# Kernel optimization log

Hardware: AMD Instinct MI355X
Metric: run time of the kernel (lower is better)

The kernel has to match this reference:

```python
import jax, jax.numpy as jnp
import numpy as np

N_E = 16384
E_DIM = 8
BETA = 0.25


def setup_inputs() -> dict:
    key = jax.random.key(0)
    k1, k2 = jax.random.split(key)
    z = jax.random.normal(k1, (4, E_DIM, 64, 64), dtype=jnp.float32)
    # nn.Embedding init: uniform(-1/n_e, 1/n_e)
    emb = jax.random.uniform(k2, (N_E, E_DIM), dtype=jnp.float32,
                             minval=-1.0 / N_E, maxval=1.0 / N_E)
    return {"z": z, "emb": emb}


def reference(z, emb):
    # z: [B, C, H, W] with C == e_dim; emb: [n_e, e_dim]
    zt = jnp.transpose(z, (0, 2, 3, 1))            # b h w c
    zf = zt.reshape(-1, E_DIM)                     # [N, e_dim]
    # squared distances: ||z||^2 + ||e||^2 - 2 z.e -> [N, n_e]
    d = (jnp.sum(zf * zf, axis=1, keepdims=True)
         + jnp.sum(emb * emb, axis=1)
         - 2.0 * jnp.einsum('nd,kd->nk', zf, emb))
    idx = jnp.argmin(d, axis=1)                    # [N]
    z_q = emb[idx].reshape(zt.shape)               # b h w c
    sg = jax.lax.stop_gradient
    # legacy loss: mean((sg(z_q)-z)^2) + beta*mean((z_q-sg(z))^2)
    loss = jnp.mean((sg(z_q) - zt) ** 2) + BETA * jnp.mean((z_q - sg(zt)) ** 2)
    # straight-through estimator
    z_q = zt + sg(z_q - zt)
    z_q = jnp.transpose(z_q, (0, 3, 1, 2))         # b c h w
    return z_q, loss, idx
```

## Files before the change

kernel.cpp:

```cpp
#include <hip/hip_runtime.h>


typedef short bf16x8  __attribute__((ext_vector_type(8)));
typedef float f32x16  __attribute__((ext_vector_type(16)));
typedef float f32x2   __attribute__((ext_vector_type(2)));

#define N_ROW 16384
#define N_E   16384
#define NSPL  32
#define SPLIT (N_E / NSPL)
#define ITER  (SPLIT / 32)
#define FIN_BLOCKS (N_ROW / 256)

static __device__ __forceinline__ unsigned short bf16_rne(float x) {
    unsigned u = __float_as_uint(x);
    unsigned r = (u >> 16) & 1u;
    return (unsigned short)((u + 0x7FFFu + r) >> 16);
}

__global__ __launch_bounds__(256) void vq_prep(const float* __restrict__ z,
                                               const float* __restrict__ emb,
                                               unsigned short* __restrict__ pz,
                                               unsigned short* __restrict__ pe_hi,
                                               float* __restrict__ Zn_arr,
                                               unsigned long long* __restrict__ key,
                                               double* __restrict__ acc,
                                               unsigned* __restrict__ done) {
    const int t = blockIdx.x * 256 + threadIdx.x;
    if (t < N_ROW) {
        const int b = t >> 12, hw = t & 4095;
        const float* zp = z + (size_t)b * 32768 + hw;
        float v[8];
#pragma unroll
        for (int c = 0; c < 8; ++c) v[c] = zp[c * 4096];
        float Zn;
        {
#pragma clang fp contract(off)
            Zn = v[0] * v[0];
#pragma unroll
            for (int c = 1; c < 8; ++c) { float q = v[c] * v[c]; Zn = Zn + q; }
        }
        unsigned hb[8], lb[8];
#pragma unroll
        for (int c = 0; c < 8; ++c) {
            hb[c] = bf16_rne(v[c]);
            float hf = __uint_as_float(hb[c] << 16);
            lb[c] = bf16_rne(v[c] - hf);
        }
        uint4 uh, ul;
        uh.x = hb[0] | (hb[1] << 16); uh.y = hb[2] | (hb[3] << 16);
        uh.z = hb[4] | (hb[5] << 16); uh.w = hb[6] | (hb[7] << 16);
        ul.x = lb[0] | (lb[1] << 16); ul.y = lb[2] | (lb[3] << 16);
        ul.z = lb[4] | (lb[5] << 16); ul.w = lb[6] | (lb[7] << 16);
        ((uint4*)pz)[(size_t)t * 2]     = uh;
        ((uint4*)pz)[(size_t)t * 2 + 1] = ul;
        Zn_arr[t] = Zn;
        key[t] = ~0ull;
        if (t == 0) { *acc = 0.0; *done = 0u; }
    } else {
        const int k = t - N_ROW;
        const float* e = emb + (size_t)k * 8;
        unsigned hb[8];
#pragma unroll
        for (int c = 0; c < 8; ++c) hb[c] = bf16_rne(e[c]);
        uint4 uh;
        uh.x = hb[0] | (hb[1] << 16); uh.y = hb[2] | (hb[3] << 16);
        uh.z = hb[4] | (hb[5] << 16); uh.w = hb[6] | (hb[7] << 16);
        ((uint4*)pe_hi)[k] = uh;
    }
}

__global__ __launch_bounds__(256, 4) void vq_maxk(const unsigned short* __restrict__ pe_hi,
                                                  const unsigned short* __restrict__ pz,
                                                  float* __restrict__ maxs) {
    __shared__ __align__(16) unsigned short se_hi[SPLIT * 8];
    const int tid = threadIdx.x, wid = tid >> 6, lane = tid & 63;
    const int rowbase = (int)(blockIdx.x >> 5) * 256;
    const int split = blockIdx.x & 31;
    const int c32 = lane & 31, hi = lane >> 5;

    bf16x8 afrag[2];
#pragma unroll
    for (int a = 0; a < 2; ++a)
        afrag[a] = *(const bf16x8*)(pz + (size_t)(rowbase + wid * 64 + a * 32 + c32) * 16 + hi * 8);

    {
        const uint4* gh = (const uint4*)(pe_hi + (size_t)split * SPLIT * 8);
        ((uint4*)se_hi)[tid]       = gh[tid];
        ((uint4*)se_hi)[tid + 256] = gh[tid + 256];
    }
    __syncthreads();

    const f32x16 zero16 = {0.f,0.f,0.f,0.f,0.f,0.f,0.f,0.f,0.f,0.f,0.f,0.f,0.f,0.f,0.f,0.f};
    f32x2 rmax2[2][8];
#pragma unroll
    for (int a = 0; a < 2; ++a)
#pragma unroll
        for (int j = 0; j < 8; ++j) rmax2[a][j] = (f32x2){-3.4e38f, -3.4e38f};

#pragma unroll 2
    for (int t = 0; t < ITER; ++t) {
        const bf16x8 bfrag = *(const bf16x8*)(se_hi + (size_t)(t * 32 + c32) * 8);
        f32x16 cc0 = __builtin_amdgcn_mfma_f32_32x32x16_bf16(afrag[0], bfrag, zero16, 0, 0, 0);
        f32x16 cc1 = __builtin_amdgcn_mfma_f32_32x32x16_bf16(afrag[1], bfrag, zero16, 0, 0, 0);
#pragma unroll
        for (int j = 0; j < 8; ++j) {
            rmax2[0][j] = __builtin_elementwise_max(rmax2[0][j], (f32x2){cc0[2*j], cc0[2*j+1]});
            rmax2[1][j] = __builtin_elementwise_max(rmax2[1][j], (f32x2){cc1[2*j], cc1[2*j+1]});
        }
    }
#pragma unroll
    for (int a = 0; a < 2; ++a)
#pragma unroll
        for (int reg = 0; reg < 16; ++reg) {
            float m = rmax2[a][reg >> 1][reg & 1];
            m = fmaxf(m, __shfl_xor(m, 1));
            m = fmaxf(m, __shfl_xor(m, 2));
            m = fmaxf(m, __shfl_xor(m, 4));
            m = fmaxf(m, __shfl_xor(m, 8));
            m = fmaxf(m, __shfl_xor(m, 16));
            if (c32 == 0) {
                const int row = rowbase + wid * 64 + a * 32 + (reg & 3) + 8 * (reg >> 2) + 4 * hi;
                maxs[(size_t)split * N_ROW + row] = m;
            }
        }
}

__global__ __launch_bounds__(256) void vq_thr(const float* __restrict__ maxs,
                                              const float* __restrict__ Zn_arr,
                                              float* __restrict__ thr) {
    const int row = blockIdx.x * 256 + threadIdx.x;
    float m = -3.4e38f;
#pragma unroll
    for (int s = 0; s < NSPL; ++s) m = fmaxf(m, maxs[(size_t)s * N_ROW + row]);
    const float Zn = Zn_arr[row];
    const float W = __builtin_fmaf(Zn, 1.5e-7f, __builtin_fmaf(__builtin_sqrtf(Zn), 6.8e-7f, 2e-7f));
    thr[row] = m - W;
}

__global__ __launch_bounds__(256, 4) void vq_coll(const float* __restrict__ z,
                                                  const float* __restrict__ emb,
                                                  const unsigned short* __restrict__ pe_hi,
                                                  const unsigned short* __restrict__ pz,
                                                  const float* __restrict__ Zn_arr,
                                                  const float* __restrict__ thr_arr,
                                                  unsigned long long* __restrict__ key) {
    __shared__ __align__(16) unsigned short se_hi[SPLIT * 8];
    __shared__ float se_z[8 * 256];
    __shared__ float sZn[256], sthr[256];
    const int tid = threadIdx.x, wid = tid >> 6, lane = tid & 63;
    const int rowbase = (int)(blockIdx.x >> 5) * 256;
    const int split = blockIdx.x & 31;
    const int c32 = lane & 31, hi = lane >> 5;

    bf16x8 afrag[2];
#pragma unroll
    for (int a = 0; a < 2; ++a)
        afrag[a] = *(const bf16x8*)(pz + (size_t)(rowbase + wid * 64 + a * 32 + c32) * 16 + hi * 8);

    {
        const uint4* gh = (const uint4*)(pe_hi + (size_t)split * SPLIT * 8);
        ((uint4*)se_hi)[tid]       = gh[tid];
        ((uint4*)se_hi)[tid + 256] = gh[tid + 256];
        const int row = rowbase + tid;
        const int b = row >> 12, hw = row & 4095;
#pragma unroll
        for (int c = 0; c < 8; ++c)
            se_z[c * 256 + tid] = z[(size_t)b * 32768 + (size_t)c * 4096 + hw];
        sZn[tid]  = Zn_arr[row];
        sthr[tid] = thr_arr[row];
    }
    __syncthreads();

    f32x2 thr2[2][8];
#pragma unroll
    for (int a = 0; a < 2; ++a) {
        const int base = wid * 64 + a * 32 + 4 * hi;
#pragma unroll
        for (int j = 0; j < 8; ++j) {
            const int r0 = base + ((2 * j) & 3) + 8 * (j >> 1);
            thr2[a][j] = (f32x2){sthr[r0], sthr[r0 + 1]};
        }
    }

    const f32x16 zero16 = {0.f,0.f,0.f,0.f,0.f,0.f,0.f,0.f,0.f,0.f,0.f,0.f,0.f,0.f,0.f,0.f};
#pragma unroll 2
    for (int t = 0; t < ITER; ++t) {
        const bf16x8 bfrag = *(const bf16x8*)(se_hi + (size_t)(t * 32 + c32) * 8);
        f32x16 cc0 = __builtin_amdgcn_mfma_f32_32x32x16_bf16(afrag[0], bfrag, zero16, 0, 0, 0);
        f32x16 cc1 = __builtin_amdgcn_mfma_f32_32x32x16_bf16(afrag[1], bfrag, zero16, 0, 0, 0);

        f32x2 dd[2][8];
#pragma unroll
        for (int j = 0; j < 8; ++j) {
            dd[0][j] = (f32x2){cc0[2*j], cc0[2*j+1]} - thr2[0][j];
            dd[1][j] = (f32x2){cc1[2*j], cc1[2*j+1]} - thr2[1][j];
        }
        f32x2 mx = dd[0][0];
#pragma unroll
        for (int j = 1; j < 8; ++j) mx = __builtin_elementwise_max(mx, dd[0][j]);
#pragma unroll
        for (int j = 0; j < 8; ++j) mx = __builtin_elementwise_max(mx, dd[1][j]);

        if (__any(fmaxf(mx.x, mx.y) >= 0.f)) {
            const int kcode = split * SPLIT + t * 32 + c32;
#pragma unroll
            for (int a = 0; a < 2; ++a) {
                f32x2 am = dd[a][0];
#pragma unroll
                for (int j = 1; j < 8; ++j) am = __builtin_elementwise_max(am, dd[a][j]);
                if (__any(fmaxf(am.x, am.y) >= 0.f)) {
#pragma unroll
                    for (int j = 0; j < 8; ++j)
#pragma unroll
                        for (int h = 0; h < 2; ++h) {
                            const float dv = dd[a][j][h];
                            if (__any(dv >= 0.f)) {
                                if (dv >= 0.f) {
                                    const int reg = 2 * j + h;
                                    const int lrow = wid * 64 + a * 32 + (reg & 3) + 8 * (reg >> 2) + 4 * hi;
                                    const float* e = emb + (size_t)kcode * 8;
                                    float dot = se_z[lrow] * e[0];
#pragma unroll
                                    for (int c = 1; c < 8; ++c)
                                        dot = __builtin_fmaf(se_z[c * 256 + lrow], e[c], dot);
                                    const float ddv = __builtin_fmaf(-2.f, dot, sZn[lrow]);
                                    unsigned u = __float_as_uint(ddv);
                                    unsigned mm = (u & 0x80000000u) ? ~u : (u | 0x80000000u);
                                    const unsigned long long kk =
                                        ((unsigned long long)mm << 32) | (unsigned)kcode;
                                    atomicMin(&key[(size_t)(rowbase + lrow)], kk);
                                }
                            }
                        }
                }
            }
        }
    }
}

__global__ __launch_bounds__(256) void vq_fin(const float* __restrict__ z,
                                              const float* __restrict__ emb,
                                              const unsigned long long* __restrict__ key,
                                              float* __restrict__ out_zq,
                                              float* __restrict__ out_idx,
                                              double* __restrict__ acc,
                                              unsigned* __restrict__ done,
                                              float* __restrict__ out_loss) {
    __shared__ float red[4];
    const int row = blockIdx.x * 256 + threadIdx.x;
    const int b = row >> 12, hw = row & 4095;
    const int kstar = (int)(unsigned)(key[row] & 0xFFFFFFFFull);
    out_idx[row] = (float)kstar;
    const float* e = emb + (size_t)kstar * 8;
    float s = 0.f;
#pragma unroll
    for (int c = 0; c < 8; ++c) {
        const size_t zoff = (size_t)b * 32768 + (size_t)c * 4096 + hw;
        const float ev = e[c];
        const float df = ev - z[zoff];
        out_zq[zoff] = ev;
        s = __builtin_fmaf(df, df, s);
    }
#pragma unroll
    for (int off = 32; off > 0; off >>= 1) s += __shfl_down(s, off, 64);
    if ((threadIdx.x & 63) == 0) red[threadIdx.x >> 6] = s;
    __syncthreads();
    if (threadIdx.x == 0) {
        double t = (double)red[0] + (double)red[1] + (double)red[2] + (double)red[3];
        atomicAdd(acc, t);
        __threadfence();
        unsigned old = atomicAdd(done, 1u);
        if (old == FIN_BLOCKS - 1) {
            double total = atomicAdd(acc, 0.0);
            float mf = (float)(total / (double)(N_ROW * 8));
            out_loss[0] = mf + 0.25f * mf;
        }
    }
}

extern "C" void kernel_launch(void* const* d_in, const int* in_sizes, int n_in,
                              void* d_out, int out_size, void* d_ws, size_t ws_size,
                              hipStream_t stream) {
    const float* z   = (const float*)d_in[0];
    const float* emb = (const float*)d_in[1];

    float* out      = (float*)d_out;
    float* out_zq   = out;
    float* out_loss = out + 131072;
    float* out_idx  = out + 131073;

    char* w = (char*)d_ws;
    double*             acc   = (double*)w;
    unsigned*           done  = (unsigned*)(w + 8);      w += 64;
    unsigned long long* key   = (unsigned long long*)w;  w += (size_t)N_ROW * 8;
    float*              Zn    = (float*)w;               w += (size_t)N_ROW * 4;
    float*              thr   = (float*)w;               w += (size_t)N_ROW * 4;
    unsigned short*     pz    = (unsigned short*)w;      w += (size_t)N_ROW * 32;
    unsigned short*     pe_hi = (unsigned short*)w;      w += (size_t)N_E * 16;
    float*              maxs  = (float*)w;               w += (size_t)N_ROW * NSPL * 4;

    vq_prep <<<dim3(128), dim3(256), 0, stream>>>(z, emb, pz, pe_hi, Zn, key, acc, done);
    vq_maxk <<<dim3((N_ROW / 256) * NSPL), dim3(256), 0, stream>>>(pe_hi, pz, maxs);
    vq_thr  <<<dim3(N_ROW / 256), dim3(256), 0, stream>>>(maxs, Zn, thr);
    vq_coll <<<dim3((N_ROW / 256) * NSPL), dim3(256), 0, stream>>>(z, emb, pe_hi, pz, Zn, thr, key);
    vq_fin  <<<dim3(FIN_BLOCKS), dim3(256), 0, stream>>>(z, emb, key, out_zq, out_idx, acc, done, out_loss);
}
```

Before: 61.24 us.

## Replace per-split max buffer with atomic max and drop threshold kernel

The max-score kernel now reduces each row's maximum straight into a global array with atomicMax on a monotone unsigned float encoding. This replaces the per-split max array and the separate threshold kernel, and the collection kernel now computes the threshold from the decoded max itself. The finalize kernel is also re-parallelized so each thread handles one output element in z's native layout rather than one row of eight strided elements. The goal is to remove a launch and the round trip of the 2 MB max buffer, at the cost of global atomic contention on the max array.

```diff
diff --git a/kernel.cpp b/kernel.cpp
--- a/kernel.cpp
+++ b/kernel.cpp
@@ -10,12 +10,20 @@
 #define NSPL  32
 #define SPLIT (N_E / NSPL)
 #define ITER  (SPLIT / 32)
-#define FIN_BLOCKS (N_ROW / 256)
+#define FIN_BLOCKS ((N_ROW * 8) / 256)
 
 static __device__ __forceinline__ unsigned short bf16_rne(float x) {
     unsigned u = __float_as_uint(x);
     unsigned r = (u >> 16) & 1u;
     return (unsigned short)((u + 0x7FFFu + r) >> 16);
+}
+static __device__ __forceinline__ unsigned mono_enc(float x) {
+    unsigned u = __float_as_uint(x);
+    return (u & 0x80000000u) ? ~u : (u | 0x80000000u);
+}
+static __device__ __forceinline__ float mono_dec(unsigned g) {
+    unsigned u = (g & 0x80000000u) ? (g & 0x7FFFFFFFu) : ~g;
+    return __uint_as_float(u);
 }
 
 __global__ __launch_bounds__(256) void vq_prep(const float* __restrict__ z,
@@ -23,6 +31,7 @@
                                                unsigned short* __restrict__ pz,
                                                unsigned short* __restrict__ pe_hi,
                                                float* __restrict__ Zn_arr,
+                                               unsigned* __restrict__ gmax,
                                                unsigned long long* __restrict__ key,
                                                double* __restrict__ acc,
                                                unsigned* __restrict__ done) {
@@ -55,6 +64,7 @@
         ((uint4*)pz)[(size_t)t * 2]     = uh;
         ((uint4*)pz)[(size_t)t * 2 + 1] = ul;
         Zn_arr[t] = Zn;
+        gmax[t] = 0u;
         key[t] = ~0ull;
         if (t == 0) { *acc = 0.0; *done = 0u; }
     } else {
@@ -72,7 +82,7 @@
 
 __global__ __launch_bounds__(256, 4) void vq_maxk(const unsigned short* __restrict__ pe_hi,
                                                   const unsigned short* __restrict__ pz,
-                                                  float* __restrict__ maxs) {
+                                                  unsigned* __restrict__ gmax) {
     __shared__ __align__(16) unsigned short se_hi[SPLIT * 8];
     const int tid = threadIdx.x, wid = tid >> 6, lane = tid & 63;
     const int rowbase = (int)(blockIdx.x >> 5) * 256;
@@ -121,21 +131,9 @@
             m = fmaxf(m, __shfl_xor(m, 16));
             if (c32 == 0) {
                 const int row = rowbase + wid * 64 + a * 32 + (reg & 3) + 8 * (reg >> 2) + 4 * hi;
-                maxs[(size_t)split * N_ROW + row] = m;
+                atomicMax(&gmax[row], mono_enc(m));
             }
         }
-}
-
-__global__ __launch_bounds__(256) void vq_thr(const float* __restrict__ maxs,
-                                              const float* __restrict__ Zn_arr,
-                                              float* __restrict__ thr) {
-    const int row = blockIdx.x * 256 + threadIdx.x;
-    float m = -3.4e38f;
-#pragma unroll
-    for (int s = 0; s < NSPL; ++s) m = fmaxf(m, maxs[(size_t)s * N_ROW + row]);
-    const float Zn = Zn_arr[row];
-    const float W = __builtin_fmaf(Zn, 1.5e-7f, __builtin_fmaf(__builtin_sqrtf(Zn), 6.8e-7f, 2e-7f));
-    thr[row] = m - W;
 }
 
 __global__ __launch_bounds__(256, 4) void vq_coll(const float* __restrict__ z,
@@ -143,7 +141,7 @@
                                                   const unsigned short* __restrict__ pe_hi,
                                                   const unsigned short* __restrict__ pz,
                                                   const float* __restrict__ Zn_arr,
-                                                  const float* __restrict__ thr_arr,
+                                                  const unsigned* __restrict__ gmax,
                                                   unsigned long long* __restrict__ key) {
     __shared__ __align__(16) unsigned short se_hi[SPLIT * 8];
     __shared__ float se_z[8 * 256];
@@ -167,8 +165,11 @@
 #pragma unroll
         for (int c = 0; c < 8; ++c)
             se_z[c * 256 + tid] = z[(size_t)b * 32768 + (size_t)c * 4096 + hw];
-        sZn[tid]  = Zn_arr[row];
-        sthr[tid] = thr_arr[row];
+        const float Zn = Zn_arr[row];
+        sZn[tid] = Zn;
+        const float W = __builtin_fmaf(Zn, 1.5e-7f,
+                          __builtin_fmaf(__builtin_sqrtf(Zn), 6.8e-7f, 2e-7f));
+        sthr[tid] = mono_dec(gmax[row]) - W;
     }
     __syncthreads();
 
@@ -225,10 +226,8 @@
                                     for (int c = 1; c < 8; ++c)
                                         dot = __builtin_fmaf(se_z[c * 256 + lrow], e[c], dot);
                                     const float ddv = __builtin_fmaf(-2.f, dot, sZn[lrow]);
-                                    unsigned u = __float_as_uint(ddv);
-                                    unsigned mm = (u & 0x80000000u) ? ~u : (u | 0x80000000u);
                                     const unsigned long long kk =
-                                        ((unsigned long long)mm << 32) | (unsigned)kcode;
+                                        ((unsigned long long)mono_enc(ddv) << 32) | (unsigned)kcode;
                                     atomicMin(&key[(size_t)(rowbase + lrow)], kk);
                                 }
                             }
@@ -248,20 +247,16 @@
                                               unsigned* __restrict__ done,
                                               float* __restrict__ out_loss) {
     __shared__ float red[4];
-    const int row = blockIdx.x * 256 + threadIdx.x;
-    const int b = row >> 12, hw = row & 4095;
+    const int i = blockIdx.x * 256 + threadIdx.x;
+    const int b = i >> 15, rem = i & 32767;
+    const int c = rem >> 12, hw = rem & 4095;
+    const int row = (b << 12) | hw;
     const int kstar = (int)(unsigned)(key[row] & 0xFFFFFFFFull);
-    out_idx[row] = (float)kstar;
-    const float* e = emb + (size_t)kstar * 8;
-    float s = 0.f;
-#pragma unroll
-    for (int c = 0; c < 8; ++c) {
-        const size_t zoff = (size_t)b * 32768 + (size_t)c * 4096 + hw;
-        const float ev = e[c];
-        const float df = ev - z[zoff];
-        out_zq[zoff] = ev;
-        s = __builtin_fmaf(df, df, s);
-    }
+    const float ev = emb[(size_t)kstar * 8 + c];
+    const float df = ev - z[i];
+    out_zq[i] = ev;
+    if (c == 0) out_idx[row] = (float)kstar;
+    float s = df * df;
 #pragma unroll
     for (int off = 32; off > 0; off >>= 1) s += __shfl_down(s, off, 64);
     if ((threadIdx.x & 63) == 0) red[threadIdx.x >> 6] = s;
@@ -294,15 +289,13 @@
     double*             acc   = (double*)w;
     unsigned*           done  = (unsigned*)(w + 8);      w += 64;
     unsigned long long* key   = (unsigned long long*)w;  w += (size_t)N_ROW * 8;
+    unsigned*           gmax  = (unsigned*)w;            w += (size_t)N_ROW * 4;
     float*              Zn    = (float*)w;               w += (size_t)N_ROW * 4;
-    float*              thr   = (float*)w;               w += (size_t)N_ROW * 4;
     unsigned short*     pz    = (unsigned short*)w;      w += (size_t)N_ROW * 32;
     unsigned short*     pe_hi = (unsigned short*)w;      w += (size_t)N_E * 16;
-    float*              maxs  = (float*)w;               w += (size_t)N_ROW * NSPL * 4;
-
-    vq_prep <<<dim3(128), dim3(256), 0, stream>>>(z, emb, pz, pe_hi, Zn, key, acc, done);
-    vq_maxk <<<dim3((N_ROW / 256) * NSPL), dim3(256), 0, stream>>>(pe_hi, pz, maxs);
-    vq_thr  <<<dim3(N_ROW / 256), dim3(256), 0, stream>>>(maxs, Zn, thr);
-    vq_coll <<<dim3((N_ROW / 256) * NSPL), dim3(256), 0, stream>>>(z, emb, pe_hi, pz, Zn, thr, key);
+
+    vq_prep <<<dim3(128), dim3(256), 0, stream>>>(z, emb, pz, pe_hi, Zn, gmax, key, acc, done);
+    vq_maxk <<<dim3((N_ROW / 256) * NSPL), dim3(256), 0, stream>>>(pe_hi, pz, gmax);
+    vq_coll <<<dim3((N_ROW / 256) * NSPL), dim3(256), 0, stream>>>(z, emb, pe_hi, pz, Zn, gmax, key);
     vq_fin  <<<dim3(FIN_BLOCKS), dim3(256), 0, stream>>>(z, emb, key, out_zq, out_idx, acc, done, out_loss);
 }
```

Measured after the change: 73.14 us. 1.19x slower.
